# Kernel tuning notes

Measured on AMD Instinct MI355X. Metric: run time of the kernel, lower is better.

## Reference

```python
import jax, jax.numpy as jnp
import numpy as np

NUM_ROUTING = 3
EPS = 1e-8


def squash(s, axis=-1):
    # v = ||s||^2/(1+||s||^2) * s/||s||
    sq = jnp.sum(s * s, axis=axis, keepdims=True)
    return sq / (1.0 + sq) * s / (jnp.sqrt(sq) + EPS)


def setup_inputs() -> dict:
    key = jax.random.key(0)
    k1, k2 = jax.random.split(key)
    batch, in_caps, in_dim = 16, 2048, 64
    num_caps, dim_caps = 64, 32
    x = jax.random.normal(k1, (batch, in_caps, in_dim), dtype=jnp.float32)
    # learned transform W[j, d, k]  (torch shape (1,num_caps,1,dim_caps,in_dim) with singletons dropped)
    W = 0.01 * jax.random.normal(k2, (num_caps, dim_caps, in_dim), dtype=jnp.float32)
    return {"x": x, "W": W}


def reference(x, W):
    # u_hat[b,j,i,d] = sum_k W[j,d,k] * x[b,i,k]
    u_hat = jnp.einsum('jdk,bik->bjid', W, x)  # (b, num_caps, in_caps, dim_caps)
    u_hat_d = jax.lax.stop_gradient(u_hat)     # routing uses detached predictions

    b = jnp.zeros(u_hat.shape[:3] + (1,), dtype=u_hat.dtype)  # (b, J, I, 1)
    for _ in range(NUM_ROUTING - 1):
        c = jax.nn.softmax(b, axis=1)                # over output capsules J
        s = jnp.sum(c * u_hat_d, axis=2)             # (b, J, D)
        v = squash(s)
        # agreement uv[b,j,i] = <u_hat_d[b,j,i,:], v[b,j,:]>
        b = b + jnp.einsum('bjid,bjd->bji', u_hat_d, v)[..., None]

    c = jax.nn.softmax(b, axis=1)
    s = jnp.sum(c * u_hat, axis=2)
    return squash(s)  # (b, num_caps, dim_caps)
```

## Files before the change

### kernel.cpp

```cpp
#include <hip/hip_runtime.h>
#include <math.h>


#define BB 16
#define II 2048
#define KK 64
#define JJ 64
#define DD 32
#define ITILE 64
#define NT 32
#define NCAPS 8
#define JPC (JJ / NCAPS)
#define JPW (JPC / 4)

#define SCRATCH_FLOATS ((KK + JJ) * 68 + 8 * 72)

#define SYNC_STRIDE 64
#define NSYNCVAR 7
#define SYNC_INTS (BB * NSYNCVAR * SYNC_STRIDE)

typedef float f32x4 __attribute__((ext_vector_type(4)));

__device__ __forceinline__ int* svar(int* sync, int b, int v) {
    return sync + ((size_t)b * NSYNCVAR + v) * SYNC_STRIDE;
}

__device__ __forceinline__ f32x4 cohload4a(const float* p) {
    f32x4 t;
    asm volatile("global_load_dwordx4 %0, %1, off sc0 sc1"
                 : "=&v"(t) : "v"(p) : "memory");
    return t;
}
__device__ __forceinline__ float cohload1a(const float* p) {
    float t;
    asm volatile("global_load_dword %0, %1, off sc0 sc1"
                 : "=&v"(t) : "v"(p) : "memory");
    return t;
}
__device__ __forceinline__ void cohwait0() {
    asm volatile("s_waitcnt vmcnt(0)" ::: "memory");
    __builtin_amdgcn_sched_barrier(0);
}
__device__ __forceinline__ void cohstore4(float* p, f32x4 v) {
    asm volatile("global_store_dwordx4 %0, %1, off sc0 sc1"
                 :: "v"(p), "v"(v) : "memory");
}
__device__ __forceinline__ void cohstore1(float* p, float v) {
    asm volatile("global_store_dword %0, %1, off sc0 sc1"
                 :: "v"(p), "v"(v) : "memory");
}
__device__ __forceinline__ void cohfence() {
    asm volatile("s_waitcnt vmcnt(0)" ::: "memory");
}

__device__ __forceinline__ void wait_ge(int* p, int val) {
    if (threadIdx.x < 64) {
        while (__hip_atomic_load(p, __ATOMIC_RELAXED, __HIP_MEMORY_SCOPE_AGENT) < val)
            __builtin_amdgcn_s_sleep(8);
    }
    __syncthreads();
}

template <int MODE>
__device__ __forceinline__ void caps_tail(int b, int chunk,
                                          const float* __restrict__ W,
                                          const float* __restrict__ ypb,
                                          float* __restrict__ wvb,
                                          float* __restrict__ out,
                                          float* scratch) {
    const int tid = threadIdx.x;
    const int w = tid >> 6, lane = tid & 63;
    float* W_sm = scratch + w * (DD * 68);
    float* y_sm = scratch + 4 * (DD * 68) + w * KK;
    float* v_sm = scratch + 4 * (DD * 68) + 4 * KK + w * DD;
    const int kq = lane & 15, th = lane >> 4;

    if (MODE == 0) {
        f32x4 vb[8];
        #pragma unroll
        for (int n = 0; n < 8; ++n)
            vb[n] = cohload4a(ypb + (th + n * 4) * KK + kq * 4);
        cohwait0();
        float ax = 0.f, ay = 0.f, az = 0.f, aw = 0.f;
        #pragma unroll
        for (int n = 0; n < 8; ++n) {
            ax += vb[n][0]; ay += vb[n][1]; az += vb[n][2]; aw += vb[n][3];
        }
        ax += __shfl_xor(ax, 16, 64); ay += __shfl_xor(ay, 16, 64);
        az += __shfl_xor(az, 16, 64); aw += __shfl_xor(aw, 16, 64);
        ax += __shfl_xor(ax, 32, 64); ay += __shfl_xor(ay, 32, 64);
        az += __shfl_xor(az, 32, 64); aw += __shfl_xor(aw, 32, 64);
        if (lane < 16)
            *(float4*)&y_sm[kq * 4] = make_float4(ax * (1.f / 64.f), ay * (1.f / 64.f),
                                                  az * (1.f / 64.f), aw * (1.f / 64.f));
    }

    #pragma unroll
    for (int jj = 0; jj < JPW; ++jj) {
        const int j = chunk * JPC + w * JPW + jj;
        const float* Wp = W + (size_t)j * DD * KK;
        #pragma unroll
        for (int rr = 0; rr < 8; ++rr) {
            const int idx = rr * 64 + lane;
            const int d = idx >> 4, kq2 = idx & 15;
            *(float4*)&W_sm[d * 68 + kq2 * 4] = *(const float4*)(Wp + d * KK + kq2 * 4);
        }

        const size_t widx = (size_t)j * KK + lane;
        float wvold = 0.f;
        if (MODE != 0) {
            f32x4 vb[8];
            #pragma unroll
            for (int n = 0; n < 8; ++n)
                vb[n] = cohload4a(ypb + ((size_t)(th + n * 4) * JJ + j) * KK + kq * 4);
            if (MODE == 1) wvold = cohload1a(wvb + widx);
            cohwait0();
            float ax = 0.f, ay = 0.f, az = 0.f, aw = 0.f;
            #pragma unroll
            for (int n = 0; n < 8; ++n) {
                ax += vb[n][0]; ay += vb[n][1]; az += vb[n][2]; aw += vb[n][3];
            }
            ax += __shfl_xor(ax, 16, 64); ay += __shfl_xor(ay, 16, 64);
            az += __shfl_xor(az, 16, 64); aw += __shfl_xor(aw, 16, 64);
            ax += __shfl_xor(ax, 32, 64); ay += __shfl_xor(ay, 32, 64);
            az += __shfl_xor(az, 32, 64); aw += __shfl_xor(aw, 32, 64);
            if (lane < 16) *(float4*)&y_sm[kq * 4] = make_float4(ax, ay, az, aw);
        }

        const int d = lane & 31;
        const int kh = (lane >> 5) * 32;
        float sv = 0.f;
        #pragma unroll
        for (int kk2 = 0; kk2 < 8; ++kk2) {
            const float4 wr = *(const float4*)&W_sm[d * 68 + kh + kk2 * 4];
            const float4 yr = *(const float4*)&y_sm[kh + kk2 * 4];
            sv += wr.x * yr.x + wr.y * yr.y + wr.z * yr.z + wr.w * yr.w;
        }
        sv += __shfl_xor(sv, 32, 64);
        float ps = sv * sv;
        #pragma unroll
        for (int m = 1; m < 32; m <<= 1) ps += __shfl_xor(ps, m, 64);
        const float f = ps / ((1.f + ps) * (sqrtf(ps) + 1e-8f));

        if (MODE == 2) {
            if (lane < DD) out[((size_t)b * JJ + j) * DD + lane] = sv * f;
        } else {
            if (lane < DD) v_sm[lane] = sv * f;
            float a = 0.f;
            #pragma unroll
            for (int dd = 0; dd < DD; ++dd) a += W_sm[dd * 68 + lane] * v_sm[dd];
            if (MODE == 1) a += wvold;
            cohstore1(wvb + widx, a);
        }
    }
}

__device__ __forceinline__ void route_pass(const float* __restrict__ wvb,
                                           float* __restrict__ ypt,
                                           float (*x_smT)[68], float* scratch) {
    const int tid = threadIdx.x;
    float (*wv_smT)[68] = (float (*)[68])scratch;
    float (*uv_smT)[68] = (float (*)[68])(scratch + KK * 68);
    float (*red)[72]    = (float (*)[72])(scratch + (KK + JJ) * 68);

    {
        f32x4 vb[4];
        #pragma unroll
        for (int n = 0; n < 4; ++n)
            vb[n] = cohload4a(wvb + (size_t)(tid + n * 256) * 4);
        cohwait0();
        #pragma unroll
        for (int n = 0; n < 4; ++n) {
            const int idx = tid + n * 256;
            const int jj = idx >> 4, kq = idx & 15;
            wv_smT[kq * 4 + 0][jj] = vb[n][0];
            wv_smT[kq * 4 + 1][jj] = vb[n][1];
            wv_smT[kq * 4 + 2][jj] = vb[n][2];
            wv_smT[kq * 4 + 3][jj] = vb[n][3];
        }
    }
    __syncthreads();

    {
        const int ib = (tid & 15) * 4, jb = (tid >> 4) * 4;
        float acc[4][4] = {};
        for (int k = 0; k < KK; ++k) {
            const float4 xv = *(const float4*)&x_smT[k][ib];
            const float4 wvv = *(const float4*)&wv_smT[k][jb];
            acc[0][0] += xv.x * wvv.x; acc[0][1] += xv.x * wvv.y;
            acc[0][2] += xv.x * wvv.z; acc[0][3] += xv.x * wvv.w;
            acc[1][0] += xv.y * wvv.x; acc[1][1] += xv.y * wvv.y;
            acc[1][2] += xv.y * wvv.z; acc[1][3] += xv.y * wvv.w;
            acc[2][0] += xv.z * wvv.x; acc[2][1] += xv.z * wvv.y;
            acc[2][2] += xv.z * wvv.z; acc[2][3] += xv.z * wvv.w;
            acc[3][0] += xv.w * wvv.x; acc[3][1] += xv.w * wvv.y;
            acc[3][2] += xv.w * wvv.z; acc[3][3] += xv.w * wvv.w;
        }
        #pragma unroll
        for (int r = 0; r < 4; ++r)
            *(float4*)&uv_smT[jb + r][ib] =
                make_float4(acc[0][r], acc[1][r], acc[2][r], acc[3][r]);
    }
    __syncthreads();

    {
        const int i = tid & 63;
        const int w = tid >> 6;
        const int j0 = w * 16;
        float e[16];
        float m = -1e30f;
        #pragma unroll
        for (int jj = 0; jj < 16; ++jj) {
            e[jj] = uv_smT[j0 + jj][i];
            m = fmaxf(m, e[jj]);
        }
        red[w][i] = m;
        __syncthreads();
        m = fmaxf(fmaxf(red[0][i], red[1][i]), fmaxf(red[2][i], red[3][i]));
        float s = 0.f;
        #pragma unroll
        for (int jj = 0; jj < 16; ++jj) {
            e[jj] = __expf(e[jj] - m);
            s += e[jj];
        }
        red[4 + w][i] = s;
        __syncthreads();
        const float inv = 1.f / (red[4][i] + red[5][i] + red[6][i] + red[7][i]);
        #pragma unroll
        for (int jj = 0; jj < 16; ++jj) uv_smT[j0 + jj][i] = e[jj] * inv;
    }
    __syncthreads();

    {
        const int a = tid & 15;
        const int kb = (tid >> 4) * 4;
        float acc[4][4] = {};
        for (int i = 0; i < ITILE; i += 4) {
            float4 xv[4];
            #pragma unroll
            for (int c = 0; c < 4; ++c) xv[c] = *(const float4*)&x_smT[kb + c][i];
            #pragma unroll
            for (int r = 0; r < 4; ++r) {
                const float4 cv = *(const float4*)&uv_smT[a + 16 * r][i];
                #pragma unroll
                for (int c = 0; c < 4; ++c)
                    acc[r][c] += cv.x * xv[c].x + cv.y * xv[c].y +
                                 cv.z * xv[c].z + cv.w * xv[c].w;
            }
        }
        #pragma unroll
        for (int r = 0; r < 4; ++r) {
            f32x4 sv;
            sv[0] = acc[r][0]; sv[1] = acc[r][1]; sv[2] = acc[r][2]; sv[3] = acc[r][3];
            cohstore4(&ypt[(a + 16 * r) * KK + kb], sv);
        }
    }
}

__global__ __launch_bounds__(256, 2) void fused_kernel(
    const float* __restrict__ x, const float* __restrict__ W,
    float* __restrict__ wv, float* __restrict__ ypart,
    float* __restrict__ out, int* __restrict__ sync) {
    const int bid = blockIdx.x;
    const int b = bid >> 5;
    const int t = bid & 31;
    const int tid = threadIdx.x;

    int* cnt0  = svar(sync, b, 0);
    int* cnt0b = svar(sync, b, 1);
    int* cnt1  = svar(sync, b, 2);
    int* cnt1b = svar(sync, b, 3);
    int* cnt2  = svar(sync, b, 4);
    int* flag1 = svar(sync, b, 5);
    int* flag2 = svar(sync, b, 6);

    float* wvb = wv + (size_t)b * JJ * KK;
    float* ypb = ypart + (size_t)b * NT * JJ * KK;

    __shared__ alignas(16) float x_smT[KK][68];
    __shared__ alignas(16) float scratch[SCRATCH_FLOATS];
    __shared__ int role_sm;

    const float4* x4 = (const float4*)(x + ((size_t)b * II + t * ITILE) * KK);
    #pragma unroll
    for (int n = 0; n < 4; ++n) {
        const int idx = tid + n * 256;
        const int i = idx >> 4, kq = idx & 15;
        const float4 v = x4[idx];
        x_smT[kq * 4 + 0][i] = v.x;
        x_smT[kq * 4 + 1][i] = v.y;
        x_smT[kq * 4 + 2][i] = v.z;
        x_smT[kq * 4 + 3][i] = v.w;
    }
    __syncthreads();

    {
        const int w = tid >> 6, lane = tid & 63;
        const int kk = lane >> 2, q = lane & 3;
        const int k = w * 16 + kk;
        float s = 0.f;
        #pragma unroll
        for (int m = 0; m < 4; ++m) {
            const float4 v = *(const float4*)&x_smT[k][q * 16 + m * 4];
            s += v.x + v.y + v.z + v.w;
        }
        s += __shfl_xor(s, 1, 64);
        s += __shfl_xor(s, 2, 64);
        if (q == 0) cohstore1(&ypb[t * KK + k], s);
    }
    cohfence();
    __syncthreads();
    if (tid == 0)
        role_sm = __hip_atomic_fetch_add(&cnt0[0], 1, __ATOMIC_RELAXED, __HIP_MEMORY_SCOPE_AGENT);
    __syncthreads();
    const int r0 = role_sm;

    if (r0 >= NT - NCAPS) {
        wait_ge(cnt0, NT);
        caps_tail<0>(b, r0 - (NT - NCAPS), W, ypb, wvb, out, scratch);
        cohfence();
        __syncthreads();
        if (tid == 0 &&
            __hip_atomic_fetch_add(&cnt0b[0], 1, __ATOMIC_RELAXED, __HIP_MEMORY_SCOPE_AGENT) == NCAPS - 1)
            __hip_atomic_store(&flag1[0], 1, __ATOMIC_RELAXED, __HIP_MEMORY_SCOPE_AGENT);
    }
    wait_ge(flag1, 1);

    route_pass(wvb, ypb + (size_t)t * JJ * KK, x_smT, scratch);

    cohfence();
    __syncthreads();
    if (tid == 0)
        role_sm = __hip_atomic_fetch_add(&cnt1[0], 1, __ATOMIC_RELAXED, __HIP_MEMORY_SCOPE_AGENT);
    __syncthreads();
    const int r1 = role_sm;

    if (r1 >= NT - NCAPS) {
        wait_ge(cnt1, NT);
        caps_tail<1>(b, r1 - (NT - NCAPS), W, ypb, wvb, out, scratch);
        cohfence();
        __syncthreads();
        if (tid == 0 &&
            __hip_atomic_fetch_add(&cnt1b[0], 1, __ATOMIC_RELAXED, __HIP_MEMORY_SCOPE_AGENT) == NCAPS - 1)
            __hip_atomic_store(&flag2[0], 1, __ATOMIC_RELAXED, __HIP_MEMORY_SCOPE_AGENT);
    }
    wait_ge(flag2, 1);

    route_pass(wvb, ypb + (size_t)t * JJ * KK, x_smT, scratch);

    cohfence();
    __syncthreads();
    if (tid == 0)
        role_sm = __hip_atomic_fetch_add(&cnt2[0], 1, __ATOMIC_RELAXED, __HIP_MEMORY_SCOPE_AGENT);
    __syncthreads();
    const int r2 = role_sm;

    if (r2 >= NT - NCAPS) {
        wait_ge(cnt2, NT);
        caps_tail<2>(b, r2 - (NT - NCAPS), W, ypb, wvb, out, scratch);
    }
}

extern "C" void kernel_launch(void* const* d_in, const int* in_sizes, int n_in,
                              void* d_out, int out_size, void* d_ws, size_t ws_size,
                              hipStream_t stream) {
    (void)in_sizes; (void)n_in; (void)out_size; (void)ws_size;
    const float* x = (const float*)d_in[0];
    const float* W = (const float*)d_in[1];
    float* out = (float*)d_out;
    float* ws = (float*)d_ws;

    float* wv = ws;
    float* ypart = ws + 65536;
    int* sync = (int*)(ws + 65536 + 2097152);

    hipMemsetAsync(sync, 0, SYNC_INTS * sizeof(int), stream);
    fused_kernel<<<dim3(BB * NT), dim3(256), 0, stream>>>(x, W, wv, ypart, out, sync);
}
```

Baseline: 100.3 us.

## Spread capsule phase across all blocks with per-block phase flags and register-held W

Replaces the scheme where the last 8 arriving blocks per batch did the capsule squash/W^T v work with one where all 32 blocks each handle 2 output capsules. Each block keeps its W slice in registers for the whole kernel and keeps the running wv in a register instead of reloading it. The atomic counters and flags are replaced by per-block phase slots polled with a wave-wide all-check. This spreads the serial tail work across more blocks and removes atomics. In exchange every block must wait at every barrier, and register pressure goes up.

```diff
diff --git a/kernel.cpp b/kernel.cpp
--- a/kernel.cpp
+++ b/kernel.cpp
@@ -9,21 +9,18 @@
 #define DD 32
 #define ITILE 64
 #define NT 32
-#define NCAPS 8
-#define JPC (JJ / NCAPS)
-#define JPW (JPC / 4)
 
 #define SCRATCH_FLOATS ((KK + JJ) * 68 + 8 * 72)
 
-#define SYNC_STRIDE 64
-#define NSYNCVAR 7
-#define SYNC_INTS (BB * NSYNCVAR * SYNC_STRIDE)
+#define PH_YBAR   1
+#define PH_CAPS0  2
+#define PH_ROUTE1 3
+#define PH_CAPS1  4
+#define PH_ROUTE2 5
+
+#define SYNC_INTS (BB * 64)
 
 typedef float f32x4 __attribute__((ext_vector_type(4)));
-
-__device__ __forceinline__ int* svar(int* sync, int b, int v) {
-    return sync + ((size_t)b * NSYNCVAR + v) * SYNC_STRIDE;
-}
 
 __device__ __forceinline__ f32x4 cohload4a(const float* p) {
     f32x4 t;
@@ -31,8 +28,8 @@
                  : "=&v"(t) : "v"(p) : "memory");
     return t;
 }
-__device__ __forceinline__ float cohload1a(const float* p) {
-    float t;
+__device__ __forceinline__ int cohload1ia(const int* p) {
+    int t;
     asm volatile("global_load_dword %0, %1, off sc0 sc1"
                  : "=&v"(t) : "v"(p) : "memory");
     return t;
@@ -49,109 +46,139 @@
     asm volatile("global_store_dword %0, %1, off sc0 sc1"
                  :: "v"(p), "v"(v) : "memory");
 }
+__device__ __forceinline__ void cohstore1i(int* p, int v) {
+    asm volatile("global_store_dword %0, %1, off sc0 sc1"
+                 :: "v"(p), "v"(v) : "memory");
+}
 __device__ __forceinline__ void cohfence() {
     asm volatile("s_waitcnt vmcnt(0)" ::: "memory");
 }
 
-__device__ __forceinline__ void wait_ge(int* p, int val) {
+__device__ __forceinline__ void set_phase(int* slot, int phase) {
+    if (threadIdx.x == 0) cohstore1i(slot, phase);
+}
+__device__ __forceinline__ void wait_all(const int* done_b, int phase) {
     if (threadIdx.x < 64) {
-        while (__hip_atomic_load(p, __ATOMIC_RELAXED, __HIP_MEMORY_SCOPE_AGENT) < val)
-            __builtin_amdgcn_s_sleep(8);
+        const int* p = done_b + (threadIdx.x & 31);
+        for (;;) {
+            int v = cohload1ia(p);
+            cohwait0();
+            if (__all(v >= phase)) break;
+            __builtin_amdgcn_s_sleep(4);
+        }
     }
     __syncthreads();
 }
 
 template <int MODE>
-__device__ __forceinline__ void caps_tail(int b, int chunk,
-                                          const float* __restrict__ W,
-                                          const float* __restrict__ ypb,
-                                          float* __restrict__ wvb,
-                                          float* __restrict__ out,
-                                          float* scratch) {
+__device__ __forceinline__ void caps_phase(
+    int b, int j0, float4 w0, float4 w1, float4 w2, float4 w3,
+    const float* __restrict__ ypb, float* __restrict__ wvb,
+    float* __restrict__ out, float* scratch, float& wv_reg) {
     const int tid = threadIdx.x;
-    const int w = tid >> 6, lane = tid & 63;
-    float* W_sm = scratch + w * (DD * 68);
-    float* y_sm = scratch + 4 * (DD * 68) + w * KK;
-    float* v_sm = scratch + 4 * (DD * 68) + 4 * KK + w * DD;
-    const int kq = lane & 15, th = lane >> 4;
-
-    if (MODE == 0) {
-        f32x4 vb[8];
-        #pragma unroll
-        for (int n = 0; n < 8; ++n)
-            vb[n] = cohload4a(ypb + (th + n * 4) * KK + kq * 4);
+    const int wave = tid >> 6, lane = tid & 63;
+    const int jr = tid >> 7, rem = tid & 127;
+
+    float* y_sm   = scratch;
+    float* wvp_sm = scratch + 128;
+    float* sq_sm  = scratch + 384;
+
+    {
+        const int jw = wave >> 1;
+        const int khalf = (wave & 1) * 32;
+        const int kq8 = lane & 7, th = lane >> 3;
+        f32x4 vb[4];
+        if (MODE == 0) {
+            #pragma unroll
+            for (int n = 0; n < 4; ++n)
+                vb[n] = cohload4a(ypb + (size_t)(th + n * 8) * KK + khalf + kq8 * 4);
+        } else {
+            const int jA = j0 + jw;
+            #pragma unroll
+            for (int n = 0; n < 4; ++n)
+                vb[n] = cohload4a(ypb + ((size_t)(th + n * 8) * JJ + jA) * KK + khalf + kq8 * 4);
+        }
         cohwait0();
-        float ax = 0.f, ay = 0.f, az = 0.f, aw = 0.f;
-        #pragma unroll
-        for (int n = 0; n < 8; ++n) {
-            ax += vb[n][0]; ay += vb[n][1]; az += vb[n][2]; aw += vb[n][3];
-        }
-        ax += __shfl_xor(ax, 16, 64); ay += __shfl_xor(ay, 16, 64);
-        az += __shfl_xor(az, 16, 64); aw += __shfl_xor(aw, 16, 64);
-        ax += __shfl_xor(ax, 32, 64); ay += __shfl_xor(ay, 32, 64);
-        az += __shfl_xor(az, 32, 64); aw += __shfl_xor(aw, 32, 64);
-        if (lane < 16)
-            *(float4*)&y_sm[kq * 4] = make_float4(ax * (1.f / 64.f), ay * (1.f / 64.f),
-                                                  az * (1.f / 64.f), aw * (1.f / 64.f));
-    }
-
+        float a0 = vb[0][0] + vb[1][0] + vb[2][0] + vb[3][0];
+        float a1 = vb[0][1] + vb[1][1] + vb[2][1] + vb[3][1];
+        float a2 = vb[0][2] + vb[1][2] + vb[2][2] + vb[3][2];
+        float a3 = vb[0][3] + vb[1][3] + vb[2][3] + vb[3][3];
+        #pragma unroll
+        for (int m = 8; m <= 32; m <<= 1) {
+            a0 += __shfl_xor(a0, m, 64);
+            a1 += __shfl_xor(a1, m, 64);
+            a2 += __shfl_xor(a2, m, 64);
+            a3 += __shfl_xor(a3, m, 64);
+        }
+        if (MODE == 0) {
+            a0 *= (1.f / 64.f); a1 *= (1.f / 64.f);
+            a2 *= (1.f / 64.f); a3 *= (1.f / 64.f);
+        }
+        if (th == 0)
+            *(float4*)&y_sm[jw * 64 + khalf + kq8 * 4] = make_float4(a0, a1, a2, a3);
+    }
+    __syncthreads();
+
+    const int d = rem >> 2, kq4 = rem & 3;
+    float sv;
+    {
+        const float* yb = y_sm + jr * 64 + kq4 * 16;
+        const float4 y0 = *(const float4*)(yb + 0);
+        const float4 y1 = *(const float4*)(yb + 4);
+        const float4 y2 = *(const float4*)(yb + 8);
+        const float4 y3 = *(const float4*)(yb + 12);
+        sv = w0.x * y0.x + w0.y * y0.y + w0.z * y0.z + w0.w * y0.w
+           + w1.x * y1.x + w1.y * y1.y + w1.z * y1.z + w1.w * y1.w
+           + w2.x * y2.x + w2.y * y2.y + w2.z * y2.z + w2.w * y2.w
+           + w3.x * y3.x + w3.y * y3.y + w3.z * y3.z + w3.w * y3.w;
+        sv += __shfl_xor(sv, 1, 64);
+        sv += __shfl_xor(sv, 2, 64);
+    }
+
+    float ps = sv * sv;
+    ps += __shfl_xor(ps, 4, 64);
+    ps += __shfl_xor(ps, 8, 64);
+    ps += __shfl_xor(ps, 16, 64);
+    ps += __shfl_xor(ps, 32, 64);
+    if (lane == 0) sq_sm[jr * 2 + (wave & 1)] = ps;
+    __syncthreads();
+    ps = sq_sm[jr * 2] + sq_sm[jr * 2 + 1];
+    const float f = ps / ((1.f + ps) * (sqrtf(ps) + 1e-8f));
+
+    if (MODE == 2) {
+        if (kq4 == 0) out[((size_t)b * JJ + j0 + jr) * DD + d] = sv * f;
+        return;
+    }
+
+    const float vv = sv * f;
+    float c[16];
+    {
+        const float4 ww[4] = {w0, w1, w2, w3};
+        #pragma unroll
+        for (int q = 0; q < 4; ++q) {
+            c[q * 4 + 0] = ww[q].x * vv;
+            c[q * 4 + 1] = ww[q].y * vv;
+            c[q * 4 + 2] = ww[q].z * vv;
+            c[q * 4 + 3] = ww[q].w * vv;
+        }
+    }
     #pragma unroll
-    for (int jj = 0; jj < JPW; ++jj) {
-        const int j = chunk * JPC + w * JPW + jj;
-        const float* Wp = W + (size_t)j * DD * KK;
-        #pragma unroll
-        for (int rr = 0; rr < 8; ++rr) {
-            const int idx = rr * 64 + lane;
-            const int d = idx >> 4, kq2 = idx & 15;
-            *(float4*)&W_sm[d * 68 + kq2 * 4] = *(const float4*)(Wp + d * KK + kq2 * 4);
-        }
-
-        const size_t widx = (size_t)j * KK + lane;
-        float wvold = 0.f;
-        if (MODE != 0) {
-            f32x4 vb[8];
-            #pragma unroll
-            for (int n = 0; n < 8; ++n)
-                vb[n] = cohload4a(ypb + ((size_t)(th + n * 4) * JJ + j) * KK + kq * 4);
-            if (MODE == 1) wvold = cohload1a(wvb + widx);
-            cohwait0();
-            float ax = 0.f, ay = 0.f, az = 0.f, aw = 0.f;
-            #pragma unroll
-            for (int n = 0; n < 8; ++n) {
-                ax += vb[n][0]; ay += vb[n][1]; az += vb[n][2]; aw += vb[n][3];
-            }
-            ax += __shfl_xor(ax, 16, 64); ay += __shfl_xor(ay, 16, 64);
-            az += __shfl_xor(az, 16, 64); aw += __shfl_xor(aw, 16, 64);
-            ax += __shfl_xor(ax, 32, 64); ay += __shfl_xor(ay, 32, 64);
-            az += __shfl_xor(az, 32, 64); aw += __shfl_xor(aw, 32, 64);
-            if (lane < 16) *(float4*)&y_sm[kq * 4] = make_float4(ax, ay, az, aw);
-        }
-
-        const int d = lane & 31;
-        const int kh = (lane >> 5) * 32;
-        float sv = 0.f;
-        #pragma unroll
-        for (int kk2 = 0; kk2 < 8; ++kk2) {
-            const float4 wr = *(const float4*)&W_sm[d * 68 + kh + kk2 * 4];
-            const float4 yr = *(const float4*)&y_sm[kh + kk2 * 4];
-            sv += wr.x * yr.x + wr.y * yr.y + wr.z * yr.z + wr.w * yr.w;
-        }
-        sv += __shfl_xor(sv, 32, 64);
-        float ps = sv * sv;
-        #pragma unroll
-        for (int m = 1; m < 32; m <<= 1) ps += __shfl_xor(ps, m, 64);
-        const float f = ps / ((1.f + ps) * (sqrtf(ps) + 1e-8f));
-
-        if (MODE == 2) {
-            if (lane < DD) out[((size_t)b * JJ + j) * DD + lane] = sv * f;
-        } else {
-            if (lane < DD) v_sm[lane] = sv * f;
-            float a = 0.f;
-            #pragma unroll
-            for (int dd = 0; dd < DD; ++dd) a += W_sm[dd * 68 + lane] * v_sm[dd];
-            if (MODE == 1) a += wvold;
-            cohstore1(wvb + widx, a);
-        }
+    for (int m = 4; m <= 32; m <<= 1)
+        #pragma unroll
+        for (int q = 0; q < 16; ++q)
+            c[q] += __shfl_xor(c[q], m, 64);
+    if (lane < 4) {
+        float* wp = wvp_sm + jr * 128 + (wave & 1) * 64 + lane * 16;
+        #pragma unroll
+        for (int q = 0; q < 16; ++q) wp[q] = c[q];
+    }
+    __syncthreads();
+    if (rem < 64) {
+        const int k = rem;
+        float tot = wvp_sm[jr * 128 + k] + wvp_sm[jr * 128 + 64 + k];
+        if (MODE == 1) tot += wv_reg;
+        wv_reg = tot;
+        cohstore1(&wvb[(size_t)(j0 + jr) * KK + k], tot);
     }
 }
 
@@ -265,21 +292,22 @@
     const int b = bid >> 5;
     const int t = bid & 31;
     const int tid = threadIdx.x;
-
-    int* cnt0  = svar(sync, b, 0);
-    int* cnt0b = svar(sync, b, 1);
-    int* cnt1  = svar(sync, b, 2);
-    int* cnt1b = svar(sync, b, 3);
-    int* cnt2  = svar(sync, b, 4);
-    int* flag1 = svar(sync, b, 5);
-    int* flag2 = svar(sync, b, 6);
-
+    const int j0 = 2 * t;
+
+    int* done_b = sync + b * 64;
     float* wvb = wv + (size_t)b * JJ * KK;
     float* ypb = ypart + (size_t)b * NT * JJ * KK;
 
     __shared__ alignas(16) float x_smT[KK][68];
     __shared__ alignas(16) float scratch[SCRATCH_FLOATS];
-    __shared__ int role_sm;
+
+    const int jr = tid >> 7, rem = tid & 127;
+    const float* Wp = W + ((size_t)(j0 + jr) * DD + (rem >> 2)) * KK + (rem & 3) * 16;
+    const float4 w0 = *(const float4*)(Wp + 0);
+    const float4 w1 = *(const float4*)(Wp + 4);
+    const float4 w2 = *(const float4*)(Wp + 8);
+    const float4 w3 = *(const float4*)(Wp + 12);
+    float wv_reg = 0.f;
 
     const float4* x4 = (const float4*)(x + ((size_t)b * II + t * ITILE) * KK);
     #pragma unroll
@@ -308,57 +336,31 @@
         s += __shfl_xor(s, 2, 64);
         if (q == 0) cohstore1(&ypb[t * KK + k], s);
     }
-    cohfence();
-    __syncthreads();
-    if (tid == 0)
-        role_sm = __hip_atomic_fetch_add(&cnt0[0], 1, __ATOMIC_RELAXED, __HIP_MEMORY_SCOPE_AGENT);
-    __syncthreads();
-    const int r0 = role_sm;
-
-    if (r0 >= NT - NCAPS) {
-        wait_ge(cnt0, NT);
-        caps_tail<0>(b, r0 - (NT - NCAPS), W, ypb, wvb, out, scratch);
-        cohfence();
-        __syncthreads();
-        if (tid == 0 &&
-            __hip_atomic_fetch_add(&cnt0b[0], 1, __ATOMIC_RELAXED, __HIP_MEMORY_SCOPE_AGENT) == NCAPS - 1)
-            __hip_atomic_store(&flag1[0], 1, __ATOMIC_RELAXED, __HIP_MEMORY_SCOPE_AGENT);
-    }
-    wait_ge(flag1, 1);
+    cohfence(); __syncthreads();
+    set_phase(done_b + t, PH_YBAR);
+    wait_all(done_b, PH_YBAR);
+
+    caps_phase<0>(b, j0, w0, w1, w2, w3, ypb, wvb, out, scratch, wv_reg);
+    cohfence(); __syncthreads();
+    set_phase(done_b + t, PH_CAPS0);
+    wait_all(done_b, PH_CAPS0);
 
     route_pass(wvb, ypb + (size_t)t * JJ * KK, x_smT, scratch);
-
-    cohfence();
-    __syncthreads();
-    if (tid == 0)
-        role_sm = __hip_atomic_fetch_add(&cnt1[0], 1, __ATOMIC_RELAXED, __HIP_MEMORY_SCOPE_AGENT);
-    __syncthreads();
-    const int r1 = role_sm;
-
-    if (r1 >= NT - NCAPS) {
-        wait_ge(cnt1, NT);
-        caps_tail<1>(b, r1 - (NT - NCAPS), W, ypb, wvb, out, scratch);
-        cohfence();
-        __syncthreads();
-        if (tid == 0 &&
-            __hip_atomic_fetch_add(&cnt1b[0], 1, __ATOMIC_RELAXED, __HIP_MEMORY_SCOPE_AGENT) == NCAPS - 1)
-            __hip_atomic_store(&flag2[0], 1, __ATOMIC_RELAXED, __HIP_MEMORY_SCOPE_AGENT);
-    }
-    wait_ge(flag2, 1);
+    cohfence(); __syncthreads();
+    set_phase(done_b + t, PH_ROUTE1);
+    wait_all(done_b, PH_ROUTE1);
+
+    caps_phase<1>(b, j0, w0, w1, w2, w3, ypb, wvb, out, scratch, wv_reg);
+    cohfence(); __syncthreads();
+    set_phase(done_b + t, PH_CAPS1);
+    wait_all(done_b, PH_CAPS1);
 
     route_pass(wvb, ypb + (size_t)t * JJ * KK, x_smT, scratch);
-
-    cohfence();
-    __syncthreads();
-    if (tid == 0)
-        role_sm = __hip_atomic_fetch_add(&cnt2[0], 1, __ATOMIC_RELAXED, __HIP_MEMORY_SCOPE_AGENT);
-    __syncthreads();
-    const int r2 = role_sm;
-
-    if (r2 >= NT - NCAPS) {
-        wait_ge(cnt2, NT);
-        caps_tail<2>(b, r2 - (NT - NCAPS), W, ypb, wvb, out, scratch);
-    }
+    cohfence(); __syncthreads();
+    set_phase(done_b + t, PH_ROUTE2);
+    wait_all(done_b, PH_ROUTE2);
+
+    caps_phase<2>(b, j0, w0, w1, w2, w3, ypb, wvb, out, scratch, wv_reg);
 }
 
 extern "C" void kernel_launch(void* const* d_in, const int* in_sizes, int n_in,
```

After: 99.54 us. No clear change (-0.7%).
